# Optimization experiments

Measured on AMD Instinct MI355X. Metric: run time of the kernel, lower is better.

The kernel has to match this reference:

```python
import jax, jax.numpy as jnp
import numpy as np

SHIFT = 4
MARGIN = 0.15


def _shift_loss(f1, m1, f2, m2):
    # f1,f2: [B,C,H,W] float; m1,m2: [B,1,H,W] bool
    # Original repeats masks to C channels; broadcasting is equivalent,
    # but mask.sum over (1,2,3) then includes a factor of C.
    C = f1.shape[1]
    dists = []
    for i in range(2 * SHIFT + 1):
        off = -SHIFT + i
        f2r = jnp.roll(f2, off, axis=-1)
        m2r = jnp.roll(m2, off, axis=-1)
        mask = m1 & m2r                              # [B,1,H,W]
        diff = jnp.where(mask, f1 - f2r, 0.0)        # broadcast over C
        num = jnp.sum(diff * diff, axis=(1, 2, 3))   # ||.||_2^2
        den = C * jnp.sum(mask, axis=(1, 2, 3)).astype(f1.dtype) + 0.001
        dists.append(num / den)
    return jnp.min(jnp.stack(dists, axis=0), axis=0)  # min over 9 shifts -> [B]


def setup_inputs() -> dict:
    key = jax.random.key(0)
    ka, kp, kn, kma, kmp, kmn = jax.random.split(key, 6)
    B, C, H, W = 64, 16, 32, 512
    a = jax.random.normal(ka, (B, C, H, W), dtype=jnp.float32)
    p = jax.random.normal(kp, (B, C, H, W), dtype=jnp.float32)
    n = jax.random.normal(kn, (B, C, H, W), dtype=jnp.float32)
    ma = jax.random.bernoulli(kma, 0.8, (B, 1, H, W))
    mp = jax.random.bernoulli(kmp, 0.8, (B, 1, H, W))
    mn = jax.random.bernoulli(kmn, 0.8, (B, 1, H, W))
    return {"a": a, "p": p, "n": n, "ma": ma, "mp": mp, "mn": mn}


def reference(a, p, n, ma, mp, mn):
    ap_loss = _shift_loss(a, ma, p, mp)
    an_loss = _shift_loss(a, ma, n, mn)
    loss = jax.nn.relu(ap_loss - an_loss + MARGIN)
    return jnp.mean(loss)
```

## Files before the change

kernel.cpp:

```cpp
#include <hip/hip_runtime.h>

#define NB 64
#define NC 16
#define NH 32
#define NW 512
#define HW (NH * NW)
#define CHW (NC * HW)
#define NOFF 9

#define WS_NUM_AP 0
#define WS_NUM_AN 576
#define WS_CNT_AP 1152
#define WS_CNT_AN 1728
#define WS_FLOATS 2304

__device__ __forceinline__ float wave_sum_f(float v) {
#pragma unroll
    for (int o = 32; o > 0; o >>= 1) v += __shfl_down(v, o, 64);
    return v;
}

__device__ __forceinline__ int wave_sum_i(int v) {
#pragma unroll
    for (int o = 32; o > 0; o >>= 1) v += __shfl_down(v, o, 64);
    return v;
}

__global__ __launch_bounds__(256) void num_kernel(
    const float* __restrict__ a, const float* __restrict__ p,
    const float* __restrict__ n, const int* __restrict__ ma,
    const int* __restrict__ mp, const int* __restrict__ mn,
    float* __restrict__ ws)
{
    const int b = blockIdx.y;
    const int tid = blockIdx.x * 256 + threadIdx.x;
    const int pos0 = tid * 4;
    const int w0 = pos0 & (NW - 1);
    const int row = pos0 - w0;
    const int idxm = row + ((w0 - 4) & (NW - 1));
    const int idxp = row + ((w0 + 4) & (NW - 1));

    const float* A = a + (size_t)b * CHW;
    const float* P = p + (size_t)b * CHW;
    const float* N = n + (size_t)b * CHW;

    float sa2[4];
    float sp2[12], sn2[12];
    float crP[NOFF][4], crN[NOFF][4];
#pragma unroll
    for (int j = 0; j < 4; ++j) sa2[j] = 0.f;
#pragma unroll
    for (int k = 0; k < 12; ++k) { sp2[k] = 0.f; sn2[k] = 0.f; }
#pragma unroll
    for (int s = 0; s < NOFF; ++s)
#pragma unroll
        for (int j = 0; j < 4; ++j) { crP[s][j] = 0.f; crN[s][j] = 0.f; }

#pragma unroll 1
    for (int c = 0; c < NC; ++c) {
        const float* Ac = A + c * HW;
        const float* Pc = P + c * HW;
        const float* Nc = N + c * HW;

        float4 av4 = *(const float4*)(Ac + pos0);
        float pb[12], nb[12];
        *(float4*)&pb[0] = *(const float4*)(Pc + idxm);
        *(float4*)&pb[4] = *(const float4*)(Pc + pos0);
        *(float4*)&pb[8] = *(const float4*)(Pc + idxp);
        *(float4*)&nb[0] = *(const float4*)(Nc + idxm);
        *(float4*)&nb[4] = *(const float4*)(Nc + pos0);
        *(float4*)&nb[8] = *(const float4*)(Nc + idxp);
        float av[4] = {av4.x, av4.y, av4.z, av4.w};

#pragma unroll
        for (int j = 0; j < 4; ++j) sa2[j] = fmaf(av[j], av[j], sa2[j]);
#pragma unroll
        for (int k = 0; k < 12; ++k) {
            sp2[k] = fmaf(pb[k], pb[k], sp2[k]);
            sn2[k] = fmaf(nb[k], nb[k], sn2[k]);
        }
#pragma unroll
        for (int s = 0; s < NOFF; ++s) {
#pragma unroll
            for (int j = 0; j < 4; ++j) {
                const int k = j + 8 - s;
                crP[s][j] = fmaf(av[j], pb[k], crP[s][j]);
                crN[s][j] = fmaf(av[j], nb[k], crN[s][j]);
            }
        }
    }

    const int* MA = ma + b * HW;
    const int* MP = mp + b * HW;
    const int* MN = mn + b * HW;
    int4 mav = *(const int4*)(MA + pos0);
    int4 mp0 = *(const int4*)(MP + idxm);
    int4 mp1 = *(const int4*)(MP + pos0);
    int4 mp2 = *(const int4*)(MP + idxp);
    int4 mn0 = *(const int4*)(MN + idxm);
    int4 mn1 = *(const int4*)(MN + pos0);
    int4 mn2 = *(const int4*)(MN + idxp);

    int mab[4]  = {mav.x, mav.y, mav.z, mav.w};
    int mpb[12] = {mp0.x, mp0.y, mp0.z, mp0.w, mp1.x, mp1.y, mp1.z, mp1.w,
                   mp2.x, mp2.y, mp2.z, mp2.w};
    int mnb[12] = {mn0.x, mn0.y, mn0.z, mn0.w, mn1.x, mn1.y, mn1.z, mn1.w,
                   mn2.x, mn2.y, mn2.z, mn2.w};

    float s_ap[NOFF], s_an[NOFF];
    int c_ap[NOFF], c_an[NOFF];
#pragma unroll
    for (int s = 0; s < NOFF; ++s) { s_ap[s] = 0.f; s_an[s] = 0.f; c_ap[s] = 0; c_an[s] = 0; }

#pragma unroll
    for (int s = 0; s < NOFF; ++s) {
#pragma unroll
        for (int j = 0; j < 4; ++j) {
            const int k = j + 8 - s;
            const float tP = fmaf(-2.f, crP[s][j], sa2[j] + sp2[k]);
            const float tN = fmaf(-2.f, crN[s][j], sa2[j] + sn2[k]);
            const bool bp = mab[j] && mpb[k];
            const bool bn = mab[j] && mnb[k];
            s_ap[s] += bp ? tP : 0.f;
            s_an[s] += bn ? tN : 0.f;
            c_ap[s] += bp ? 1 : 0;
            c_an[s] += bn ? 1 : 0;
        }
    }

    const int lane = threadIdx.x & 63;
#pragma unroll
    for (int s = 0; s < NOFF; ++s) {
        float v = wave_sum_f(s_ap[s]);
        if (lane == 0) atomicAdd(&ws[WS_NUM_AP + b * NOFF + s], v);
        float u = wave_sum_f(s_an[s]);
        if (lane == 0) atomicAdd(&ws[WS_NUM_AN + b * NOFF + s], u);
        int ci = wave_sum_i(c_ap[s]);
        if (lane == 0) atomicAdd(&ws[WS_CNT_AP + b * NOFF + s], (float)ci);
        int cj = wave_sum_i(c_an[s]);
        if (lane == 0) atomicAdd(&ws[WS_CNT_AN + b * NOFF + s], (float)cj);
    }
}

__global__ void finish_kernel(const float* __restrict__ ws, float* __restrict__ out)
{
    const int b = threadIdx.x;
    const float* num_ap = ws + WS_NUM_AP;
    const float* num_an = ws + WS_NUM_AN;
    const float* cnt_ap = ws + WS_CNT_AP;
    const float* cnt_an = ws + WS_CNT_AN;

    float ap = 3.4e38f, an = 3.4e38f;
#pragma unroll
    for (int s = 0; s < NOFF; ++s) {
        ap = fminf(ap, num_ap[b * NOFF + s] / (16.f * cnt_ap[b * NOFF + s] + 0.001f));
        an = fminf(an, num_an[b * NOFF + s] / (16.f * cnt_an[b * NOFF + s] + 0.001f));
    }
    float loss = fmaxf(ap - an + 0.15f, 0.f);
    loss = wave_sum_f(loss);
    if (b == 0) out[0] = loss * (1.0f / 64.f);
}

extern "C" void kernel_launch(void* const* d_in, const int* in_sizes, int n_in,
                              void* d_out, int out_size, void* d_ws, size_t ws_size,
                              hipStream_t stream) {
    const float* a = (const float*)d_in[0];
    const float* p = (const float*)d_in[1];
    const float* n = (const float*)d_in[2];
    const int* ma = (const int*)d_in[3];
    const int* mp = (const int*)d_in[4];
    const int* mn = (const int*)d_in[5];
    float* ws = (float*)d_ws;
    float* out = (float*)d_out;

    hipMemsetAsync(d_ws, 0, WS_FLOATS * sizeof(float), stream);

    num_kernel<<<dim3(16, NB), 256, 0, stream>>>(a, p, n, ma, mp, mn, ws);
    finish_kernel<<<1, 64, 0, stream>>>(ws, out);
}
```

Baseline: 260.8 us.

## Split work across pair and channel-group grid dimensions to raise occupancy

Grid grows from 16x64 to 16x4x64 blocks. Each block now handles one pair (anchor-positive or anchor-negative) and one half of the channels, so it keeps far fewer accumulator registers. Launch bounds request 4 blocks per multiprocessor and the channel loop is unrolled by 2, aiming for more waves in flight to hide memory latency. In exchange, the anchor tensor and the masks are read twice, and there are more atomic adds into the workspace; only channel group 0 adds the mask counts.

```diff
diff --git a/kernel.cpp b/kernel.cpp
--- a/kernel.cpp
+++ b/kernel.cpp
@@ -26,119 +26,105 @@
     return v;
 }
 
-__global__ __launch_bounds__(256) void num_kernel(
+__global__ __launch_bounds__(256, 4) void num_kernel(
     const float* __restrict__ a, const float* __restrict__ p,
     const float* __restrict__ n, const int* __restrict__ ma,
     const int* __restrict__ mp, const int* __restrict__ mn,
     float* __restrict__ ws)
 {
-    const int b = blockIdx.y;
-    const int tid = blockIdx.x * 256 + threadIdx.x;
+    const int b    = blockIdx.z;
+    const int pair = blockIdx.y & 1;
+    const int cg   = blockIdx.y >> 1;
+    const int tid  = blockIdx.x * 256 + threadIdx.x;
     const int pos0 = tid * 4;
-    const int w0 = pos0 & (NW - 1);
-    const int row = pos0 - w0;
+    const int w0   = pos0 & (NW - 1);
+    const int row  = pos0 - w0;
     const int idxm = row + ((w0 - 4) & (NW - 1));
     const int idxp = row + ((w0 + 4) & (NW - 1));
 
-    const float* A = a + (size_t)b * CHW;
-    const float* P = p + (size_t)b * CHW;
-    const float* N = n + (size_t)b * CHW;
+    const float* A = a + (size_t)b * CHW + (size_t)cg * 8 * HW;
+    const float* F = (pair ? n : p) + (size_t)b * CHW + (size_t)cg * 8 * HW;
 
     float sa2[4];
-    float sp2[12], sn2[12];
-    float crP[NOFF][4], crN[NOFF][4];
+    float sf2[12];
+    float cr[NOFF][4];
 #pragma unroll
     for (int j = 0; j < 4; ++j) sa2[j] = 0.f;
 #pragma unroll
-    for (int k = 0; k < 12; ++k) { sp2[k] = 0.f; sn2[k] = 0.f; }
+    for (int k = 0; k < 12; ++k) sf2[k] = 0.f;
 #pragma unroll
     for (int s = 0; s < NOFF; ++s)
 #pragma unroll
-        for (int j = 0; j < 4; ++j) { crP[s][j] = 0.f; crN[s][j] = 0.f; }
+        for (int j = 0; j < 4; ++j) cr[s][j] = 0.f;
 
-#pragma unroll 1
-    for (int c = 0; c < NC; ++c) {
+#pragma unroll 2
+    for (int c = 0; c < 8; ++c) {
         const float* Ac = A + c * HW;
-        const float* Pc = P + c * HW;
-        const float* Nc = N + c * HW;
+        const float* Fc = F + c * HW;
 
         float4 av4 = *(const float4*)(Ac + pos0);
-        float pb[12], nb[12];
-        *(float4*)&pb[0] = *(const float4*)(Pc + idxm);
-        *(float4*)&pb[4] = *(const float4*)(Pc + pos0);
-        *(float4*)&pb[8] = *(const float4*)(Pc + idxp);
-        *(float4*)&nb[0] = *(const float4*)(Nc + idxm);
-        *(float4*)&nb[4] = *(const float4*)(Nc + pos0);
-        *(float4*)&nb[8] = *(const float4*)(Nc + idxp);
+        float fb[12];
+        *(float4*)&fb[0] = *(const float4*)(Fc + idxm);
+        *(float4*)&fb[4] = *(const float4*)(Fc + pos0);
+        *(float4*)&fb[8] = *(const float4*)(Fc + idxp);
         float av[4] = {av4.x, av4.y, av4.z, av4.w};
 
 #pragma unroll
         for (int j = 0; j < 4; ++j) sa2[j] = fmaf(av[j], av[j], sa2[j]);
 #pragma unroll
-        for (int k = 0; k < 12; ++k) {
-            sp2[k] = fmaf(pb[k], pb[k], sp2[k]);
-            sn2[k] = fmaf(nb[k], nb[k], sn2[k]);
-        }
+        for (int k = 0; k < 12; ++k) sf2[k] = fmaf(fb[k], fb[k], sf2[k]);
 #pragma unroll
         for (int s = 0; s < NOFF; ++s) {
 #pragma unroll
             for (int j = 0; j < 4; ++j) {
                 const int k = j + 8 - s;
-                crP[s][j] = fmaf(av[j], pb[k], crP[s][j]);
-                crN[s][j] = fmaf(av[j], nb[k], crN[s][j]);
+                cr[s][j] = fmaf(av[j], fb[k], cr[s][j]);
             }
         }
     }
 
     const int* MA = ma + b * HW;
-    const int* MP = mp + b * HW;
-    const int* MN = mn + b * HW;
+    const int* M2 = (pair ? mn : mp) + b * HW;
     int4 mav = *(const int4*)(MA + pos0);
-    int4 mp0 = *(const int4*)(MP + idxm);
-    int4 mp1 = *(const int4*)(MP + pos0);
-    int4 mp2 = *(const int4*)(MP + idxp);
-    int4 mn0 = *(const int4*)(MN + idxm);
-    int4 mn1 = *(const int4*)(MN + pos0);
-    int4 mn2 = *(const int4*)(MN + idxp);
+    int4 mf0 = *(const int4*)(M2 + idxm);
+    int4 mf1 = *(const int4*)(M2 + pos0);
+    int4 mf2 = *(const int4*)(M2 + idxp);
 
     int mab[4]  = {mav.x, mav.y, mav.z, mav.w};
-    int mpb[12] = {mp0.x, mp0.y, mp0.z, mp0.w, mp1.x, mp1.y, mp1.z, mp1.w,
-                   mp2.x, mp2.y, mp2.z, mp2.w};
-    int mnb[12] = {mn0.x, mn0.y, mn0.z, mn0.w, mn1.x, mn1.y, mn1.z, mn1.w,
-                   mn2.x, mn2.y, mn2.z, mn2.w};
+    int mfb[12] = {mf0.x, mf0.y, mf0.z, mf0.w, mf1.x, mf1.y, mf1.z, mf1.w,
+                   mf2.x, mf2.y, mf2.z, mf2.w};
 
-    float s_ap[NOFF], s_an[NOFF];
-    int c_ap[NOFF], c_an[NOFF];
+    float sx[NOFF];
+    int   cx[NOFF];
 #pragma unroll
-    for (int s = 0; s < NOFF; ++s) { s_ap[s] = 0.f; s_an[s] = 0.f; c_ap[s] = 0; c_an[s] = 0; }
+    for (int s = 0; s < NOFF; ++s) { sx[s] = 0.f; cx[s] = 0; }
 
 #pragma unroll
     for (int s = 0; s < NOFF; ++s) {
 #pragma unroll
         for (int j = 0; j < 4; ++j) {
             const int k = j + 8 - s;
-            const float tP = fmaf(-2.f, crP[s][j], sa2[j] + sp2[k]);
-            const float tN = fmaf(-2.f, crN[s][j], sa2[j] + sn2[k]);
-            const bool bp = mab[j] && mpb[k];
-            const bool bn = mab[j] && mnb[k];
-            s_ap[s] += bp ? tP : 0.f;
-            s_an[s] += bn ? tN : 0.f;
-            c_ap[s] += bp ? 1 : 0;
-            c_an[s] += bn ? 1 : 0;
+            const float t = fmaf(-2.f, cr[s][j], sa2[j] + sf2[k]);
+            const bool bm = mab[j] && mfb[k];
+            sx[s] += bm ? t : 0.f;
+            cx[s] += bm ? 1 : 0;
         }
     }
 
     const int lane = threadIdx.x & 63;
+    float* numws = ws + (pair ? WS_NUM_AN : WS_NUM_AP) + b * NOFF;
+    float* cntws = ws + (pair ? WS_CNT_AN : WS_CNT_AP) + b * NOFF;
 #pragma unroll
     for (int s = 0; s < NOFF; ++s) {
-        float v = wave_sum_f(s_ap[s]);
-        if (lane == 0) atomicAdd(&ws[WS_NUM_AP + b * NOFF + s], v);
-        float u = wave_sum_f(s_an[s]);
-        if (lane == 0) atomicAdd(&ws[WS_NUM_AN + b * NOFF + s], u);
-        int ci = wave_sum_i(c_ap[s]);
-        if (lane == 0) atomicAdd(&ws[WS_CNT_AP + b * NOFF + s], (float)ci);
-        int cj = wave_sum_i(c_an[s]);
-        if (lane == 0) atomicAdd(&ws[WS_CNT_AN + b * NOFF + s], (float)cj);
+        float v = wave_sum_f(sx[s]);
+        if (lane == 0) atomicAdd(numws + s, v);
+    }
+    if (cg == 0) {
+#pragma unroll
+        for (int s = 0; s < NOFF; ++s) {
+            int ci = wave_sum_i(cx[s]);
+            if (lane == 0) atomicAdd(cntws + s, (float)ci);
+        }
     }
 }
 
@@ -175,6 +161,6 @@
 
     hipMemsetAsync(d_ws, 0, WS_FLOATS * sizeof(float), stream);
 
-    num_kernel<<<dim3(16, NB), 256, 0, stream>>>(a, p, n, ma, mp, mn, ws);
+    num_kernel<<<dim3(16, 4, NB), 256, 0, stream>>>(a, p, n, ma, mp, mn, ws);
     finish_kernel<<<1, 64, 0, stream>>>(ws, out);
 }
```

Measured after the change: 315.3 us. 1.21x slower.
